# Kernel tuning notes

Measured on AMD Instinct MI355X. Metric: run time of the kernel, lower is better.

Reference implementation:

```python
import jax, jax.numpy as jnp
import numpy as np


def setup_inputs() -> dict:
    key = jax.random.key(0)
    k1, k2, k3, k4 = jax.random.split(key, 4)
    d_in, d_out, B, T = 1024, 1024, 4, 2048
    scale = 1.0 / np.sqrt(d_in)
    return {
        "x": jax.random.normal(k1, (B, T, d_in), dtype=jnp.float32),
        "Wq": jax.random.normal(k2, (d_in, d_out), dtype=jnp.float32) * scale,
        "Wk": jax.random.normal(k3, (d_in, d_out), dtype=jnp.float32) * scale,
        "Wv": jax.random.normal(k4, (d_in, d_out), dtype=jnp.float32) * scale,
    }


def reference(x, Wq, Wk, Wv):
    # x: [B, T, d_in]; Wq/Wk/Wv: [d_in, d_out] (Linear, bias=False)
    q = jnp.einsum("btd,de->bte", x, Wq)
    k = jnp.einsum("btd,de->bte", x, Wk)
    v = jnp.einsum("btd,de->bte", x, Wv)
    d_out = k.shape[-1]
    scores = jnp.einsum("bqe,bke->bqk", q, k)  # [B, T, T]
    T = x.shape[1]
    causal = jnp.triu(jnp.ones((T, T), dtype=bool), k=1)  # True above diagonal
    scores = jnp.where(causal[None, :, :], -jnp.inf, scores)
    # original divides after masking; -inf stays -inf so math is identical
    att = jax.nn.softmax(scores / jnp.sqrt(jnp.asarray(d_out, scores.dtype)), axis=-1)
    # dropout p=0.0 -> identity
    return jnp.einsum("bqk,bke->bqe", att, v)
```

## Files before the change

### kernel.cpp

```cpp
#include <hip/hip_runtime.h>
#include <stdint.h>
#include <math.h>

typedef unsigned short u16;
typedef __bf16 bf16x8 __attribute__((ext_vector_type(8)));
typedef float f32x4 __attribute__((ext_vector_type(4)));

enum { M_QKV = 0, M_SCORE = 1, M_PV = 2 };

__device__ __forceinline__ u16 f2bf(float f) {
    union { float f; unsigned int u; } a; a.f = f;
    unsigned int u = a.u;
    u += 0x7FFFu + ((u >> 16) & 1u);
    return (u16)(u >> 16);
}

__device__ __forceinline__ void async_load16(const void* g, void* l) {
    __builtin_amdgcn_global_load_lds(
        (const __attribute__((address_space(1))) void*)g,
        (__attribute__((address_space(3))) void*)l,
        16, 0, 0);
}

template<int MODE, int TBM>
__global__ __launch_bounds__(256)
void gemm_bt(const u16* __restrict__ A, long long sAb,
             const u16* __restrict__ Bt, long long sBb,
             void* __restrict__ Cv, long long sCb,
             float* __restrict__ rowsum,
             int M, int N, int K, float kfac)
{
    constexpr int KB  = 64;
    constexpr int NI  = TBM / 32;
    constexpr int ACH = TBM / 32;
    constexpr int BCH = 4;

    int bm, bn;
    if (MODE == M_SCORE) {
        const int idx = blockIdx.x;
        int w = (int)sqrtf((float)idx + 0.5f);
        while (w * w > idx) --w;
        while ((w + 1) * (w + 1) <= idx) ++w;
        if (idx < w * w + w) { bm = 2 * w - 1; bn = idx - w * w; }
        else                 { bm = 2 * w;     bn = idx - (w * w + w); }
    } else {
        bn = blockIdx.x; bm = blockIdx.y;
    }
    const int bz = blockIdx.z;
    A  += (size_t)bz * sAb;
    Bt += (size_t)bz * sBb;

    const int tid  = threadIdx.x;
    const int lane = tid & 63;
    const int wv   = tid >> 6;
    const int wm   = wv >> 1;
    const int wn   = wv & 1;

    __shared__ __attribute__((aligned(16))) u16 As[TBM * KB];
    __shared__ __attribute__((aligned(16))) u16 Bs[128 * KB];

    f32x4 acc[NI][4] = {};

    const int rowA0 = bm * TBM, rowB0 = bn * 128;
    const int lrow  = lane >> 3;
    const int lslot = lane & 7;
    const int sg    = (lslot ^ lrow) * 8;

    int kEnd = K;
    if (MODE == M_PV) { int ke = (bm + 1) * TBM; kEnd = ke < K ? ke : K; }

    const int lm   = lane & 15;
    const int quad = lane >> 4;
    const int rx   = lm & 7;

    for (int k0 = 0; k0 < kEnd; k0 += KB) {
        #pragma unroll
        for (int c = 0; c < ACH; ++c) {
            const int cc  = wv * ACH + c;
            const int row = cc * 8 + lrow;
            async_load16(&A[(size_t)(rowA0 + row) * K + k0 + sg], &As[cc * 512 + lane * 8]);
        }
        #pragma unroll
        for (int c = 0; c < BCH; ++c) {
            const int cc  = wv * BCH + c;
            const int row = cc * 8 + lrow;
            async_load16(&Bt[(size_t)(rowB0 + row) * K + k0 + sg], &Bs[cc * 512 + lane * 8]);
        }
        __syncthreads();

        #pragma unroll
        for (int h = 0; h < 2; ++h) {
            const int sl = (((h * 4 + quad) ^ rx) * 8);
            bf16x8 af[NI], bfr[4];
            #pragma unroll
            for (int i = 0; i < NI; ++i)
                af[i] = *reinterpret_cast<const bf16x8*>(
                    &As[(wm * (TBM / 2) + i * 16 + lm) * KB + sl]);
            #pragma unroll
            for (int j = 0; j < 4; ++j)
                bfr[j] = *reinterpret_cast<const bf16x8*>(
                    &Bs[(wn * 64 + j * 16 + lm) * KB + sl]);
            #pragma unroll
            for (int i = 0; i < NI; ++i)
                #pragma unroll
                for (int j = 0; j < 4; ++j)
                    acc[i][j] = __builtin_amdgcn_mfma_f32_16x16x32_bf16(af[i], bfr[j], acc[i][j], 0, 0, 0);
        }
        __syncthreads();
    }

    if (MODE == M_QKV) {
        u16* C = (u16*)Cv + (size_t)(bn >> 3) * sCb;
        #pragma unroll
        for (int i = 0; i < NI; ++i)
            #pragma unroll
            for (int j = 0; j < 4; ++j) {
                const int r0 = rowA0 + wm * (TBM / 2) + i * 16 + quad * 4;
                const int c0 = (rowB0 + wn * 64 + j * 16 + lm) & 1023;
                #pragma unroll
                for (int g = 0; g < 4; ++g)
                    C[(size_t)(r0 + g) * 1024 + c0] = f2bf(acc[i][j][g]);
            }
    } else if (MODE == M_SCORE) {
        u16* E = (u16*)Cv + (size_t)bz * sCb;
        float rs[NI][4];
        #pragma unroll
        for (int i = 0; i < NI; ++i)
            #pragma unroll
            for (int g = 0; g < 4; ++g) rs[i][g] = 0.f;
        #pragma unroll
        for (int i = 0; i < NI; ++i)
            #pragma unroll
            for (int j = 0; j < 4; ++j) {
                const int r0 = rowA0 + wm * (TBM / 2) + i * 16 + quad * 4;
                const int c  = rowB0 + wn * 64 + j * 16 + lm;
                #pragma unroll
                for (int g = 0; g < 4; ++g) {
                    const int r = r0 + g;
                    float e = (c <= r) ? exp2f(acc[i][j][g] * kfac) : 0.f;
                    E[(size_t)r * N + c] = f2bf(e);
                    rs[i][g] += e;
                }
            }
        #pragma unroll
        for (int i = 0; i < NI; ++i)
            #pragma unroll
            for (int g = 0; g < 4; ++g) {
                float v = rs[i][g];
                v += __shfl_xor(v, 1); v += __shfl_xor(v, 2);
                v += __shfl_xor(v, 4); v += __shfl_xor(v, 8);
                rs[i][g] = v;
            }
        if (lm == 0) {
            #pragma unroll
            for (int i = 0; i < NI; ++i)
                #pragma unroll
                for (int g = 0; g < 4; ++g) {
                    const int r = rowA0 + wm * (TBM / 2) + i * 16 + quad * 4 + g;
                    atomicAdd(&rowsum[(size_t)bz * M + r], rs[i][g]);
                }
        }
    } else {
        float* C = (float*)Cv + (size_t)bz * sCb;
        #pragma unroll
        for (int i = 0; i < NI; ++i) {
            const int r0 = rowA0 + wm * (TBM / 2) + i * 16 + quad * 4;
            float inv[4];
            #pragma unroll
            for (int g = 0; g < 4; ++g)
                inv[g] = 1.f / rowsum[(size_t)bz * M + r0 + g];
            #pragma unroll
            for (int j = 0; j < 4; ++j) {
                const int c0 = rowB0 + wn * 64 + j * 16 + lm;
                #pragma unroll
                for (int g = 0; g < 4; ++g)
                    C[(size_t)(r0 + g) * N + c0] = acc[i][j][g] * inv[g];
            }
        }
    }
}

__global__ __launch_bounds__(256)
void cast_x(const float* __restrict__ x, u16* __restrict__ o, long long n)
{
    long long i = ((long long)blockIdx.x * blockDim.x + threadIdx.x) * 8;
    if (i >= n) return;
    const float4 a = *(const float4*)(x + i);
    const float4 b = *(const float4*)(x + i + 4);
    union { u16 u[8]; float4 v; } r;
    r.u[0] = f2bf(a.x); r.u[1] = f2bf(a.y); r.u[2] = f2bf(a.z); r.u[3] = f2bf(a.w);
    r.u[4] = f2bf(b.x); r.u[5] = f2bf(b.y); r.u[6] = f2bf(b.z); r.u[7] = f2bf(b.w);
    *(float4*)(o + i) = r.v;
}

__global__ __launch_bounds__(256)
void castT_w3(const float* __restrict__ W0, const float* __restrict__ W1,
              const float* __restrict__ W2, u16* __restrict__ Wt, int D)
{
    const float* W = blockIdx.z == 0 ? W0 : (blockIdx.z == 1 ? W1 : W2);
    u16* dst = Wt + (size_t)blockIdx.z * D * D;
    __shared__ u16 t[32][33];
    const int c0 = blockIdx.x * 32, r0 = blockIdx.y * 32;
    const int tx = threadIdx.x & 31, ty = threadIdx.x >> 5;
    #pragma unroll
    for (int s = 0; s < 32; s += 8)
        t[ty + s][tx] = f2bf(W[(size_t)(r0 + ty + s) * D + c0 + tx]);
    __syncthreads();
    #pragma unroll
    for (int s = 0; s < 32; s += 8)
        dst[(size_t)(c0 + ty + s) * D + r0 + tx] = t[tx][ty + s];
}

__global__ __launch_bounds__(256)
void transpose_b(const u16* __restrict__ V, long long sVb,
                 u16* __restrict__ Vt, long long sVtb, int rows, int cols)
{
    V  += (size_t)blockIdx.z * sVb;
    Vt += (size_t)blockIdx.z * sVtb;
    __shared__ u16 t[32][33];
    const int c0 = blockIdx.x * 32, r0 = blockIdx.y * 32;
    const int tx = threadIdx.x & 31, ty = threadIdx.x >> 5;
    #pragma unroll
    for (int s = 0; s < 32; s += 8)
        t[ty + s][tx] = V[(size_t)(r0 + ty + s) * cols + c0 + tx];
    __syncthreads();
    #pragma unroll
    for (int s = 0; s < 32; s += 8)
        Vt[(size_t)(c0 + ty + s) * rows + r0 + tx] = t[tx][ty + s];
}

extern "C" void kernel_launch(void* const* d_in, const int* in_sizes, int n_in,
                              void* d_out, int out_size, void* d_ws, size_t ws_size,
                              hipStream_t stream)
{
    const int B = 4, T = 2048, D = 1024;
    const float* x  = (const float*)d_in[0];
    const float* Wq = (const float*)d_in[1];
    const float* Wk = (const float*)d_in[2];
    const float* Wv = (const float*)d_in[3];
    float* out = (float*)d_out;

    const size_t nX = (size_t)B * T * D;
    u16* Xb = (u16*)d_ws;
    u16* Wt = Xb + nX;
    u16* Q  = Wt + 3 * (size_t)D * D;
    u16* Kb = Q + nX;
    u16* Vb = Kb + nX;
    u16* Vt = Vb + nX;
    char* rest = (char*)(Vt + nX);
    const size_t fixed   = (size_t)((char*)rest - (char*)d_ws);
    const size_t perb_E  = (size_t)T * T * 2;
    const size_t perb_rs = (size_t)T * 4;
    const bool full = ws_size >= fixed + (size_t)B * (perb_E + perb_rs);
    const int nb = full ? B : 1;
    u16*   E  = (u16*)rest;
    float* RS = (float*)(E + nb * (size_t)T * T);

    const float kfac = 1.4426950408889634f / 32.0f;
    const int nTri64 = 272;

    hipMemsetAsync(RS, 0, (size_t)nb * T * 4, stream);

    cast_x<<<dim3((unsigned)(nX / (8 * 256))), 256, 0, stream>>>(x, Xb, (long long)nX);
    castT_w3<<<dim3(D / 32, D / 32, 3), 256, 0, stream>>>(Wq, Wk, Wv, Wt, D);

    gemm_bt<M_QKV, 128><<<dim3(3 * D / 128, (B * T) / 128, 1), 256, 0, stream>>>(
        Xb, 0, Wt, 0, Q, (long long)nX, nullptr, B * T, 3 * D, D, 0.f);

    if (full) {
        gemm_bt<M_SCORE, 64><<<dim3(nTri64, 1, B), 256, 0, stream>>>(
            Q, (long long)T * D, Kb, (long long)T * D, E, (long long)T * T, RS,
            T, T, D, kfac);
        transpose_b<<<dim3(D / 32, T / 32, B), 256, 0, stream>>>(
            Vb, (long long)T * D, Vt, (long long)D * T, T, D);
        gemm_bt<M_PV, 64><<<dim3(D / 128, T / 64, B), 256, 0, stream>>>(
            E, (long long)T * T, Vt, (long long)D * T, out, (long long)T * D, RS,
            T, D, T, 0.f);
    } else {
        for (int b = 0; b < B; ++b) {
            const size_t ob = (size_t)b * T * D;
            if (b) hipMemsetAsync(RS, 0, (size_t)T * 4, stream);
            gemm_bt<M_SCORE, 64><<<dim3(nTri64, 1, 1), 256, 0, stream>>>(
                Q + ob, 0, Kb + ob, 0, E, 0, RS, T, T, D, kfac);
            transpose_b<<<dim3(D / 32, T / 32, 1), 256, 0, stream>>>(
                Vb + ob, 0, Vt, 0, T, D);
            gemm_bt<M_PV, 64><<<dim3(D / 128, T / 64, 1), 256, 0, stream>>>(
                E, 0, Vt, 0, out + ob, 0, RS, T, D, T, 0.f);
        }
    }
}
```

Baseline: 247.4 us.

## Merge prep, score+V-transpose launches and reverse PV block order

Folds the x cast, weight cast-transpose and rowsum zeroing into one prep kernel, replacing a memset and two launches. The V transpose now runs as extra blocks inside the score kernel so it overlaps the triangular score GEMM. The PV kernel issues its longest-K row blocks first to improve tail balance. Shared memory in the score kernel now also holds the transpose tile, which may lower occupancy slightly.

```diff
diff --git a/kernel.cpp b/kernel.cpp
--- a/kernel.cpp
+++ b/kernel.cpp
@@ -23,32 +23,16 @@
 }
 
 template<int MODE, int TBM>
-__global__ __launch_bounds__(256)
-void gemm_bt(const u16* __restrict__ A, long long sAb,
-             const u16* __restrict__ Bt, long long sBb,
-             void* __restrict__ Cv, long long sCb,
-             float* __restrict__ rowsum,
-             int M, int N, int K, float kfac)
+__device__ __forceinline__ void gemm_core(
+    const u16* __restrict__ A, const u16* __restrict__ Bt,
+    void* __restrict__ Cv, float* __restrict__ rowsum,
+    int bm, int bn, int bz, int M, int N, int K, float kfac,
+    u16* As, u16* Bs)
 {
     constexpr int KB  = 64;
     constexpr int NI  = TBM / 32;
     constexpr int ACH = TBM / 32;
     constexpr int BCH = 4;
-
-    int bm, bn;
-    if (MODE == M_SCORE) {
-        const int idx = blockIdx.x;
-        int w = (int)sqrtf((float)idx + 0.5f);
-        while (w * w > idx) --w;
-        while ((w + 1) * (w + 1) <= idx) ++w;
-        if (idx < w * w + w) { bm = 2 * w - 1; bn = idx - w * w; }
-        else                 { bm = 2 * w;     bn = idx - (w * w + w); }
-    } else {
-        bn = blockIdx.x; bm = blockIdx.y;
-    }
-    const int bz = blockIdx.z;
-    A  += (size_t)bz * sAb;
-    Bt += (size_t)bz * sBb;
 
     const int tid  = threadIdx.x;
     const int lane = tid & 63;
@@ -56,9 +40,6 @@
     const int wm   = wv >> 1;
     const int wn   = wv & 1;
 
-    __shared__ __attribute__((aligned(16))) u16 As[TBM * KB];
-    __shared__ __attribute__((aligned(16))) u16 Bs[128 * KB];
-
     f32x4 acc[NI][4] = {};
 
     const int rowA0 = bm * TBM, rowB0 = bn * 128;
@@ -110,7 +91,7 @@
     }
 
     if (MODE == M_QKV) {
-        u16* C = (u16*)Cv + (size_t)(bn >> 3) * sCb;
+        u16* C = (u16*)Cv + (size_t)(bn >> 3) * ((size_t)M * 1024);
         #pragma unroll
         for (int i = 0; i < NI; ++i)
             #pragma unroll
@@ -122,7 +103,7 @@
                     C[(size_t)(r0 + g) * 1024 + c0] = f2bf(acc[i][j][g]);
             }
     } else if (MODE == M_SCORE) {
-        u16* E = (u16*)Cv + (size_t)bz * sCb;
+        u16* E = (u16*)Cv + (size_t)bz * ((size_t)M * N);
         float rs[NI][4];
         #pragma unroll
         for (int i = 0; i < NI; ++i)
@@ -161,7 +142,7 @@
                 }
         }
     } else {
-        float* C = (float*)Cv + (size_t)bz * sCb;
+        float* C = (float*)Cv + (size_t)bz * ((size_t)M * N);
         #pragma unroll
         for (int i = 0; i < NI; ++i) {
             const int r0 = rowA0 + wm * (TBM / 2) + i * 16 + quad * 4;
@@ -181,52 +162,104 @@
 }
 
 __global__ __launch_bounds__(256)
-void cast_x(const float* __restrict__ x, u16* __restrict__ o, long long n)
-{
-    long long i = ((long long)blockIdx.x * blockDim.x + threadIdx.x) * 8;
-    if (i >= n) return;
-    const float4 a = *(const float4*)(x + i);
-    const float4 b = *(const float4*)(x + i + 4);
-    union { u16 u[8]; float4 v; } r;
-    r.u[0] = f2bf(a.x); r.u[1] = f2bf(a.y); r.u[2] = f2bf(a.z); r.u[3] = f2bf(a.w);
-    r.u[4] = f2bf(b.x); r.u[5] = f2bf(b.y); r.u[6] = f2bf(b.z); r.u[7] = f2bf(b.w);
-    *(float4*)(o + i) = r.v;
+void k_qkv(const u16* __restrict__ Xb, const u16* __restrict__ Wt,
+           u16* __restrict__ Q, int M, int N, int K)
+{
+    __shared__ __attribute__((aligned(16))) u16 As[128 * 64];
+    __shared__ __attribute__((aligned(16))) u16 Bs[128 * 64];
+    gemm_core<M_QKV, 128>(Xb, Wt, Q, nullptr, blockIdx.y, blockIdx.x, 0,
+                          M, N, K, 0.f, As, Bs);
 }
 
 __global__ __launch_bounds__(256)
-void castT_w3(const float* __restrict__ W0, const float* __restrict__ W1,
-              const float* __restrict__ W2, u16* __restrict__ Wt, int D)
-{
-    const float* W = blockIdx.z == 0 ? W0 : (blockIdx.z == 1 ? W1 : W2);
-    u16* dst = Wt + (size_t)blockIdx.z * D * D;
-    __shared__ u16 t[32][33];
-    const int c0 = blockIdx.x * 32, r0 = blockIdx.y * 32;
-    const int tx = threadIdx.x & 31, ty = threadIdx.x >> 5;
-    #pragma unroll
-    for (int s = 0; s < 32; s += 8)
-        t[ty + s][tx] = f2bf(W[(size_t)(r0 + ty + s) * D + c0 + tx]);
-    __syncthreads();
-    #pragma unroll
-    for (int s = 0; s < 32; s += 8)
-        dst[(size_t)(c0 + ty + s) * D + r0 + tx] = t[tx][ty + s];
+void k_score_vt(const u16* __restrict__ Q, const u16* __restrict__ Kb,
+                u16* __restrict__ E, float* __restrict__ rowsum,
+                const u16* __restrict__ Vb, u16* __restrict__ Vt,
+                int T, int D, float kfac, int nTri)
+{
+    __shared__ __attribute__((aligned(16))) u16 As[64 * 64];
+    __shared__ __attribute__((aligned(16))) u16 Bs[128 * 64];
+    __shared__ u16 tt[32][33];
+    const int bz = blockIdx.z;
+
+    if ((int)blockIdx.x < nTri) {
+        const int idx = blockIdx.x;
+        int w = (int)sqrtf((float)idx + 0.5f);
+        while (w * w > idx) --w;
+        while ((w + 1) * (w + 1) <= idx) ++w;
+        int bm, bn;
+        if (idx < w * w + w) { bm = 2 * w - 1; bn = idx - w * w; }
+        else                 { bm = 2 * w;     bn = idx - (w * w + w); }
+        gemm_core<M_SCORE, 64>(Q + (size_t)bz * T * D, Kb + (size_t)bz * T * D,
+                               E, rowsum, bm, bn, bz, T, T, D, kfac, As, Bs);
+    } else {
+        const int t  = blockIdx.x - nTri;
+        const int cx = t & 31;
+        const int cy = t >> 5;
+        const u16* V = Vb + (size_t)bz * T * D;
+        u16*      Vo = Vt + (size_t)bz * D * T;
+        const int c0 = cx * 32, r0 = cy * 32;
+        const int tx = threadIdx.x & 31, ty = threadIdx.x >> 5;
+        #pragma unroll
+        for (int s = 0; s < 32; s += 8)
+            tt[ty + s][tx] = V[(size_t)(r0 + ty + s) * D + c0 + tx];
+        __syncthreads();
+        #pragma unroll
+        for (int s = 0; s < 32; s += 8)
+            Vo[(size_t)(c0 + ty + s) * T + r0 + tx] = tt[tx][ty + s];
+    }
 }
 
 __global__ __launch_bounds__(256)
-void transpose_b(const u16* __restrict__ V, long long sVb,
-                 u16* __restrict__ Vt, long long sVtb, int rows, int cols)
-{
-    V  += (size_t)blockIdx.z * sVb;
-    Vt += (size_t)blockIdx.z * sVtb;
-    __shared__ u16 t[32][33];
-    const int c0 = blockIdx.x * 32, r0 = blockIdx.y * 32;
-    const int tx = threadIdx.x & 31, ty = threadIdx.x >> 5;
-    #pragma unroll
-    for (int s = 0; s < 32; s += 8)
-        t[ty + s][tx] = V[(size_t)(r0 + ty + s) * cols + c0 + tx];
-    __syncthreads();
-    #pragma unroll
-    for (int s = 0; s < 32; s += 8)
-        Vt[(size_t)(c0 + ty + s) * rows + r0 + tx] = t[tx][ty + s];
+void k_pv(const u16* __restrict__ E, const u16* __restrict__ Vt,
+          float* __restrict__ out, const float* __restrict__ rowsum,
+          int T, int D)
+{
+    __shared__ __attribute__((aligned(16))) u16 As[64 * 64];
+    __shared__ __attribute__((aligned(16))) u16 Bs[128 * 64];
+    const int bz = blockIdx.z;
+    const int bm = (gridDim.y - 1) - blockIdx.y;
+    gemm_core<M_PV, 64>(E + (size_t)bz * T * T, Vt + (size_t)bz * D * T,
+                        out, (float*)rowsum, bm, blockIdx.x, bz,
+                        T, D, T, 0.f, As, Bs);
+}
+
+__global__ __launch_bounds__(256)
+void k_prep(const float* __restrict__ x,
+            const float* __restrict__ W0, const float* __restrict__ W1,
+            const float* __restrict__ W2,
+            u16* __restrict__ Xb, u16* __restrict__ Wt, float* __restrict__ RS,
+            int D, int nCX, int nW)
+{
+    const int bx = blockIdx.x;
+    if (bx < nCX) {
+        long long i = ((long long)bx * 256 + threadIdx.x) * 8;
+        const float4 a = *(const float4*)(x + i);
+        const float4 b = *(const float4*)(x + i + 4);
+        union { u16 u[8]; float4 v; } r;
+        r.u[0] = f2bf(a.x); r.u[1] = f2bf(a.y); r.u[2] = f2bf(a.z); r.u[3] = f2bf(a.w);
+        r.u[4] = f2bf(b.x); r.u[5] = f2bf(b.y); r.u[6] = f2bf(b.z); r.u[7] = f2bf(b.w);
+        *(float4*)(Xb + i) = r.v;
+    } else if (bx < nCX + nW) {
+        __shared__ u16 t[32][33];
+        const int w  = bx - nCX;
+        const int z  = w >> 10;
+        const int rm = w & 1023;
+        const float* W = z == 0 ? W0 : (z == 1 ? W1 : W2);
+        u16* dst = Wt + (size_t)z * D * D;
+        const int c0 = (rm & 31) * 32, r0 = (rm >> 5) * 32;
+        const int tx = threadIdx.x & 31, ty = threadIdx.x >> 5;
+        #pragma unroll
+        for (int s = 0; s < 32; s += 8)
+            t[ty + s][tx] = f2bf(W[(size_t)(r0 + ty + s) * D + c0 + tx]);
+        __syncthreads();
+        #pragma unroll
+        for (int s = 0; s < 32; s += 8)
+            dst[(size_t)(c0 + ty + s) * D + r0 + tx] = t[tx][ty + s];
+    } else {
+        const int t = bx - nCX - nW;
+        ((float4*)RS)[t * 256 + threadIdx.x] = float4{0.f, 0.f, 0.f, 0.f};
+    }
 }
 
 extern "C" void kernel_launch(void* const* d_in, const int* in_sizes, int n_in,
@@ -258,34 +291,30 @@
 
     const float kfac = 1.4426950408889634f / 32.0f;
     const int nTri64 = 272;
-
-    hipMemsetAsync(RS, 0, (size_t)nb * T * 4, stream);
-
-    cast_x<<<dim3((unsigned)(nX / (8 * 256))), 256, 0, stream>>>(x, Xb, (long long)nX);
-    castT_w3<<<dim3(D / 32, D / 32, 3), 256, 0, stream>>>(Wq, Wk, Wv, Wt, D);
-
-    gemm_bt<M_QKV, 128><<<dim3(3 * D / 128, (B * T) / 128, 1), 256, 0, stream>>>(
-        Xb, 0, Wt, 0, Q, (long long)nX, nullptr, B * T, 3 * D, D, 0.f);
+    const int nCX = (int)(nX / (8 * 256));
+    const int nW  = 3 * (D / 32) * (D / 32);
+    const int nRS = (nb * T) / (4 * 256);
 
     if (full) {
-        gemm_bt<M_SCORE, 64><<<dim3(nTri64, 1, B), 256, 0, stream>>>(
-            Q, (long long)T * D, Kb, (long long)T * D, E, (long long)T * T, RS,
-            T, T, D, kfac);
-        transpose_b<<<dim3(D / 32, T / 32, B), 256, 0, stream>>>(
-            Vb, (long long)T * D, Vt, (long long)D * T, T, D);
-        gemm_bt<M_PV, 64><<<dim3(D / 128, T / 64, B), 256, 0, stream>>>(
-            E, (long long)T * T, Vt, (long long)D * T, out, (long long)T * D, RS,
-            T, D, T, 0.f);
+        k_prep<<<dim3(nCX + nW + nRS), 256, 0, stream>>>(
+            x, Wq, Wk, Wv, Xb, Wt, RS, D, nCX, nW);
+        k_qkv<<<dim3(3 * D / 128, (B * T) / 128), 256, 0, stream>>>(
+            Xb, Wt, Q, B * T, 3 * D, D);
+        k_score_vt<<<dim3(nTri64 + (D / 32) * (T / 32), 1, B), 256, 0, stream>>>(
+            Q, Kb, E, RS, Vb, Vt, T, D, kfac, nTri64);
+        k_pv<<<dim3(D / 128, T / 64, B), 256, 0, stream>>>(E, Vt, out, RS, T, D);
     } else {
+        k_prep<<<dim3(nCX + nW + nRS), 256, 0, stream>>>(
+            x, Wq, Wk, Wv, Xb, Wt, RS, D, nCX, nW);
+        k_qkv<<<dim3(3 * D / 128, (B * T) / 128), 256, 0, stream>>>(
+            Xb, Wt, Q, B * T, 3 * D, D);
         for (int b = 0; b < B; ++b) {
             const size_t ob = (size_t)b * T * D;
             if (b) hipMemsetAsync(RS, 0, (size_t)T * 4, stream);
-            gemm_bt<M_SCORE, 64><<<dim3(nTri64, 1, 1), 256, 0, stream>>>(
-                Q + ob, 0, Kb + ob, 0, E, 0, RS, T, T, D, kfac);
-            transpose_b<<<dim3(D / 32, T / 32, 1), 256, 0, stream>>>(
-                Vb + ob, 0, Vt, 0, T, D);
-            gemm_bt<M_PV, 64><<<dim3(D / 128, T / 64, 1), 256, 0, stream>>>(
-                E, 0, Vt, 0, out + ob, 0, RS, T, D, T, 0.f);
-        }
-    }
-}
+            k_score_vt<<<dim3(nTri64 + (D / 32) * (T / 32), 1, 1), 256, 0, stream>>>(
+                Q + ob, Kb + ob, E, RS, Vb + ob, Vt, T, D, kfac, nTri64);
+            k_pv<<<dim3(D / 128, T / 64, 1), 256, 0, stream>>>(
+                E, Vt, out + ob, RS, T, D);
+        }
+    }
+}
```

Result: no change. 246.2 us (-0.5%).
